# Kernel tuning notes

Measured on AMD Instinct MI355X. Metric: run time of the kernel, lower is better.

## Reference

```python
import jax, jax.numpy as jnp
import numpy as np

B, T, DE, DD, A, FN, FS = 32, 2000, 512, 1024, 128, 32, 16
TEMPERATURE = 1.0


def setup_inputs() -> dict:
    key = jax.random.key(0)
    ks = jax.random.split(key, 10)
    input_enc = jax.random.normal(ks[0], (B, T, DE), dtype=jnp.float32)
    # lengths in [T//2, T] so no zero-length utterances
    enc_lengths = jax.random.randint(ks[1], (B,), T // 2, T + 1, dtype=jnp.int32)
    input_dec = jax.random.normal(ks[2], (B, DD), dtype=jnp.float32)
    # prev_att: previous-step attention weights (masked, normalized)
    prev_att = jax.random.uniform(ks[3], (B, T), dtype=jnp.float32)
    pad = jnp.arange(T)[None, :] >= enc_lengths[:, None]
    prev_att = jnp.where(pad, 0.0, prev_att)
    prev_att = prev_att / jnp.sum(prev_att, axis=1, keepdims=True)
    # parameters
    conv_w = jax.random.normal(ks[4], (FN, 1, 2 * FS + 1), dtype=jnp.float32) * 0.1  # [out,in,k]
    enc_w = jax.random.normal(ks[5], (A, DE), dtype=jnp.float32) * 0.04
    dec_w = jax.random.normal(ks[6], (A, DD), dtype=jnp.float32) * 0.03
    att_w = jax.random.normal(ks[7], (A, FN), dtype=jnp.float32) * 0.17
    att_b = jnp.zeros((A,), dtype=jnp.float32)
    out_w = jax.random.normal(ks[8], (1, A), dtype=jnp.float32) * 0.09
    return dict(input_enc=input_enc, enc_lengths=enc_lengths, input_dec=input_dec,
                prev_att=prev_att, conv_w=conv_w, enc_w=enc_w, dec_w=dec_w,
                att_w=att_w, att_b=att_b, out_w=out_w)


def reference(input_enc, enc_lengths, input_dec, prev_att,
              conv_w, enc_w, dec_w, att_w, att_b, out_w):
    b, t, _ = input_enc.shape
    fs = (conv_w.shape[-1] - 1) // 2  # 'same' padding
    # padding mask: True at padded positions t >= length
    mask = jnp.arange(t)[None, :] >= enc_lengths[:, None]  # [B,T]
    # location features: Conv1d over prev attention, 1 -> FN channels, same length
    conv = jax.lax.conv_general_dilated(
        prev_att[:, None, :], conv_w, window_strides=(1,),
        padding=[(fs, fs)], dimension_numbers=("NCH", "OIH", "NCH"))  # [B,FN,T]
    loc_feat = conv.transpose(0, 2, 1)  # [B,T,FN]
    projected_att = loc_feat @ att_w.T + att_b        # [B,T,A]
    projected_enc = input_enc @ enc_w.T               # [B,T,A]
    projected_dec = (input_dec @ dec_w.T)[:, None, :]  # [B,1,A]
    score = jnp.squeeze(jnp.tanh(projected_att + projected_enc + projected_dec) @ out_w.T, -1)  # [B,T]
    score = jnp.where(mask, -jnp.inf, score)
    att_weight = jax.nn.softmax(TEMPERATURE * score, axis=1)  # [B,T]
    context = jnp.einsum("btd,bt->bd", input_enc, att_weight)  # [B,DE]
    return context, att_weight
```

## Files before the change

### kernel.cpp

```cpp
#include <hip/hip_runtime.h>
#include <hip/hip_bf16.h>
#include <math.h>

#define B_ 32
#define T_ 2000
#define DE_ 512
#define DD_ 1024
#define A_ 128
#define FN_ 32
#define FS_ 16
#define KW_ (2*FS_+1)

typedef __bf16 bf16x8 __attribute__((ext_vector_type(8)));
typedef __bf16 bf16x4 __attribute__((ext_vector_type(4)));
typedef float f32x4 __attribute__((ext_vector_type(4)));

#define BT 64
#define LSTR 40

__device__ __forceinline__ void load_lds16(const void* g, void* l) {
    __builtin_amdgcn_global_load_lds(
        (const __attribute__((address_space(1))) unsigned int*)g,
        (__attribute__((address_space(3))) unsigned int*)l, 16, 0, 0);
}

__device__ __forceinline__ bf16x8 cvt8v(f32x4 x, f32x4 y) {
    bf16x8 o;
    o[0] = (__bf16)x[0]; o[1] = (__bf16)x[1]; o[2] = (__bf16)x[2]; o[3] = (__bf16)x[3];
    o[4] = (__bf16)y[0]; o[5] = (__bf16)y[1]; o[6] = (__bf16)y[2]; o[7] = (__bf16)y[3];
    return o;
}

__global__ __launch_bounds__(256) void prep_kernel(
    const float* __restrict__ enc_w, const float* __restrict__ att_w,
    const float* __restrict__ input_dec, const float* __restrict__ dec_w,
    const float* __restrict__ att_b,
    __bf16* __restrict__ enc_bf, __bf16* __restrict__ att_bf,
    float* __restrict__ pdec, float* __restrict__ ctx_un )
{
    int bx = blockIdx.x, tid = threadIdx.x;
    if (bx < 64) {
        int i = bx * 256 + tid;
        float4 v = ((const float4*)enc_w)[i];
        bf16x4 o;
        o[0] = (__bf16)v.x; o[1] = (__bf16)v.y; o[2] = (__bf16)v.z; o[3] = (__bf16)v.w;
        *(bf16x4*)(enc_bf + (size_t)i * 4) = o;
        if (i < (A_ * FN_) / 4) {
            float4 w = ((const float4*)att_w)[i];
            bf16x4 p;
            p[0] = (__bf16)w.x; p[1] = (__bf16)w.y; p[2] = (__bf16)w.z; p[3] = (__bf16)w.w;
            *(bf16x4*)(att_bf + (size_t)i * 4) = p;
        }
    } else if (bx < 192) {
        int pb = bx - 64;
        int b  = pb >> 2;
        int a0 = (pb & 3) * 32;
        int al = tid >> 3;
        int kg = tid & 7;
        int a  = a0 + al;
        const float4* w = (const float4*)(dec_w + (size_t)a * DD_);
        const float4* x = (const float4*)(input_dec + (size_t)b * DD_);
        float acc = 0.f;
        #pragma unroll 8
        for (int j = 0; j < 32; j++) {
            int i4 = kg + j * 8;
            float4 wv = w[i4], xv = x[i4];
            acc += wv.x * xv.x + wv.y * xv.y + wv.z * xv.z + wv.w * xv.w;
        }
        acc += __shfl_xor(acc, 1, 64);
        acc += __shfl_xor(acc, 2, 64);
        acc += __shfl_xor(acc, 4, 64);
        if (kg == 0) pdec[b * A_ + a] = acc + att_b[a];
    } else {
        int idx = (bx - 192) * 256 + tid;
        if (idx < (B_ * DE_ + B_) / 4 + 1)
            ((float4*)ctx_un)[idx] = make_float4(0.f, 0.f, 0.f, 0.f);
    }
}

__global__ __launch_bounds__(256, 2) void score_kernel(
    const float* __restrict__ input_enc, const __bf16* __restrict__ enc_bf,
    const float* __restrict__ prev_att,  const float* __restrict__ conv_w,
    const __bf16* __restrict__ att_bf,   const float* __restrict__ pdec,
    const float* __restrict__ out_w,     const int* __restrict__ lengths,
    float* __restrict__ wbuf, float* __restrict__ ctx_un,
    float* __restrict__ denom)
{
    __shared__ __align__(16) char At[2][16384];
    __shared__ __align__(16) char Bt[2][16384];
    __shared__ __align__(16) float pa_s[BT + 2 * FS_];
    __shared__ __align__(16) __bf16 loc_s[BT * LSTR];
    __shared__ float w_s[BT];

    const int tid  = threadIdx.x;
    const int lane = tid & 63;
    const int wv   = tid >> 6;
    const int b  = blockIdx.y;
    const int t0 = blockIdx.x * BT;
    const int len = lengths[b];

    auto issueA = [&](int kc, int bufi) {
        #pragma unroll
        for (int j = 0; j < 4; j++) {
            int s  = j * 256 + tid;
            int r  = s >> 4;
            int q  = s & 15;
            int cl = q ^ (r & 15);
            int t  = t0 + r; if (t > T_ - 1) t = T_ - 1;
            load_lds16(input_enc + ((size_t)(b * T_ + t)) * DE_ + kc + cl * 4,
                       At[bufi] + j * 4096 + wv * 1024);
        }
    };
    auto issueB = [&](int kc, int bufi) {
        #pragma unroll
        for (int j = 0; j < 4; j++) {
            int s  = j * 256 + tid;
            int r  = s >> 3;
            int cp = s & 7;
            int c  = cp ^ (r & 7);
            load_lds16(enc_bf + (size_t)r * DE_ + kc + c * 8,
                       Bt[bufi] + j * 4096 + wv * 1024);
        }
    };

    issueA(0, 0);  issueB(0, 0);
    issueA(64, 1); issueB(64, 1);

    const int f    = tid & 31;
    const int rblk = tid >> 5;
    float cwr[KW_];
    #pragma unroll
    for (int k = 0; k < KW_; k++) cwr[k] = conv_w[f * KW_ + k];

    if (tid < BT + 2 * FS_) {
        int t = t0 - FS_ + tid;
        pa_s[tid] = (t >= 0 && t < T_) ? prev_att[b * T_ + t] : 0.f;
    }
    __syncthreads();

    {
        float par[40];
        #pragma unroll
        for (int j = 0; j < 10; j++)
            *(float4*)&par[j * 4] = *(const float4*)&pa_s[rblk * 8 + j * 4];
        float accv[8] = {0.f, 0.f, 0.f, 0.f, 0.f, 0.f, 0.f, 0.f};
        #pragma unroll
        for (int k = 0; k < KW_; k++) {
            float c = cwr[k];
            #pragma unroll
            for (int j = 0; j < 8; j++) accv[j] += par[j + k] * c;
        }
        #pragma unroll
        for (int j = 0; j < 8; j++)
            loc_s[(rblk * 8 + j) * LSTR + f] = (__bf16)accv[j];
    }
    __syncthreads();

    const int col  = lane & 15;
    const int grp  = lane >> 4;
    const int rowb = wv * 16 + col;
    const int sw   = (col & 7);
    const int key  = rowb & 15;

    f32x4 acc[8];
    const f32x4 zero = (f32x4){0.f, 0.f, 0.f, 0.f};

    {
        bf16x8 afrag = *(const bf16x8*)(loc_s + rowb * LSTR + grp * 8);
        #pragma unroll
        for (int i = 0; i < 8; i++) {
            bf16x8 bfrag = *(const bf16x8*)(att_bf + (size_t)(i * 16 + col) * FN_ + grp * 8);
            acc[i] = __builtin_amdgcn_mfma_f32_16x16x32_bf16(afrag, bfrag, zero, 0, 0, 0);
        }
    }

    auto compute = [&](const char* Ab, const char* Bb) {
        f32x4 v0 = *(const f32x4*)(Ab + rowb * 256 + ((grp * 2)     ^ key) * 16);
        f32x4 v1 = *(const f32x4*)(Ab + rowb * 256 + ((grp * 2 + 1) ^ key) * 16);
        f32x4 v2 = *(const f32x4*)(Ab + rowb * 256 + ((8 + grp * 2)     ^ key) * 16);
        f32x4 v3 = *(const f32x4*)(Ab + rowb * 256 + ((8 + grp * 2 + 1) ^ key) * 16);
        bf16x8 af0 = cvt8v(v0, v1);
        bf16x8 af1 = cvt8v(v2, v3);
        #pragma unroll
        for (int i = 0; i < 8; i++) {
            bf16x8 bfrag = *(const bf16x8*)(Bb + (i * 16 + col) * 128 + ((grp ^ sw) * 16));
            acc[i] = __builtin_amdgcn_mfma_f32_16x16x32_bf16(af0, bfrag, acc[i], 0, 0, 0);
        }
        #pragma unroll
        for (int i = 0; i < 8; i++) {
            bf16x8 bfrag = *(const bf16x8*)(Bb + (i * 16 + col) * 128 + (((4 + grp) ^ sw) * 16));
            acc[i] = __builtin_amdgcn_mfma_f32_16x16x32_bf16(af1, bfrag, acc[i], 0, 0, 0);
        }
    };

    #pragma unroll
    for (int it = 0; it < 8; ++it) {
        compute(At[it & 1], Bt[it & 1]);
        if (it == 7) break;
        __builtin_amdgcn_s_barrier();
        if (it + 2 < 8) {
            issueA((it + 2) * 64, it & 1);
            issueB((it + 2) * 64, it & 1);
            asm volatile("s_waitcnt vmcnt(8)" ::: "memory");
        } else {
            asm volatile("s_waitcnt vmcnt(0)" ::: "memory");
        }
        __builtin_amdgcn_s_barrier();
        __builtin_amdgcn_sched_barrier(0);
    }

    float s[4] = {0.f, 0.f, 0.f, 0.f};
    float Mabs = 0.f;
    #pragma unroll
    for (int i = 0; i < 8; i++) {
        int a = i * 16 + col;
        float ow = out_w[a];
        Mabs += fabsf(ow);
        float bias = pdec[b * A_ + a];
        #pragma unroll
        for (int r = 0; r < 4; r++) {
            float v = acc[i][r] + bias;
            v = fminf(fmaxf(v, -15.f), 15.f);
            float e = __expf(2.f * v);
            s[r] += ow * ((e - 1.f) / (e + 1.f));
        }
    }
    #pragma unroll
    for (int r = 0; r < 4; r++) {
        s[r] += __shfl_xor(s[r], 1, 64);
        s[r] += __shfl_xor(s[r], 2, 64);
        s[r] += __shfl_xor(s[r], 4, 64);
        s[r] += __shfl_xor(s[r], 8, 64);
    }
    Mabs += __shfl_xor(Mabs, 1, 64);
    Mabs += __shfl_xor(Mabs, 2, 64);
    Mabs += __shfl_xor(Mabs, 4, 64);
    Mabs += __shfl_xor(Mabs, 8, 64);

    if (col == 0) {
        #pragma unroll
        for (int r = 0; r < 4; r++) {
            int rl = wv * 16 + grp * 4 + r;
            int t = t0 + rl;
            float w = 0.f;
            if (t < len) w = __expf(s[r] - Mabs);
            w_s[rl] = w;
            if (t < T_) wbuf[b * T_ + t] = w;
        }
    }
    __syncthreads();

    if (tid < 64) {
        float w = w_s[tid];
        w += __shfl_xor(w, 1, 64);
        w += __shfl_xor(w, 2, 64);
        w += __shfl_xor(w, 4, 64);
        w += __shfl_xor(w, 8, 64);
        w += __shfl_xor(w, 16, 64);
        w += __shfl_xor(w, 32, 64);
        if (tid == 0) atomicAdd(&denom[b], w);
    }

    int n_eff = len - t0;
    if (n_eff > BT) n_eff = BT;
    if (n_eff > 0) {
        int d0 = tid * 2;
        const float* ebase = input_enc + ((size_t)(b * T_ + t0)) * DE_ + d0;
        float cx = 0.f, cy = 0.f;
        #pragma unroll 8
        for (int t = 0; t < n_eff; t++) {
            float w = w_s[t];
            float2 v = *(const float2*)(ebase + (size_t)t * DE_);
            cx += w * v.x;
            cy += w * v.y;
        }
        atomicAdd(&ctx_un[b * DE_ + d0 + 0], cx);
        atomicAdd(&ctx_un[b * DE_ + d0 + 1], cy);
    }
}

__global__ __launch_bounds__(256) void finalize_kernel(
    const float* __restrict__ wbuf, const float* __restrict__ ctx_un,
    const float* __restrict__ denom, float* __restrict__ out)
{
    int bx = blockIdx.x, tid = threadIdx.x;
    if (bx < 64) {
        int i4 = bx * 256 + tid;
        if (i4 < (B_ * T_) / 4) {
            int b = i4 / (T_ / 4);
            float inv = 1.f / denom[b];
            float4 w = ((const float4*)wbuf)[i4];
            w.x *= inv; w.y *= inv; w.z *= inv; w.w *= inv;
            ((float4*)(out + B_ * DE_))[i4] = w;
        }
    } else {
        int j = (bx - 64) * 256 + tid;
        int b = j / (DE_ / 4);
        float inv = 1.f / denom[b];
        float4 c = ((const float4*)ctx_un)[j];
        c.x *= inv; c.y *= inv; c.z *= inv; c.w *= inv;
        ((float4*)out)[j] = c;
    }
}

extern "C" void kernel_launch(void* const* d_in, const int* in_sizes, int n_in,
                              void* d_out, int out_size, void* d_ws, size_t ws_size,
                              hipStream_t stream)
{
    const float* input_enc   = (const float*)d_in[0];
    const int*   enc_lengths = (const int*)d_in[1];
    const float* input_dec   = (const float*)d_in[2];
    const float* prev_att    = (const float*)d_in[3];
    const float* conv_w      = (const float*)d_in[4];
    const float* enc_w       = (const float*)d_in[5];
    const float* dec_w       = (const float*)d_in[6];
    const float* att_w       = (const float*)d_in[7];
    const float* att_b       = (const float*)d_in[8];
    const float* out_w       = (const float*)d_in[9];

    float* out = (float*)d_out;
    char* ws = (char*)d_ws;
    float*  pdec   = (float*)ws;
    float*  wbuf   = (float*)(ws + 16384);
    __bf16* enc_bf = (__bf16*)(ws + 272384);
    __bf16* att_bf = (__bf16*)(ws + 403456);
    float*  ctx_un = (float*)(ws + 411648);
    float*  denom  = (float*)(ws + 477184);

    prep_kernel<<<209, 256, 0, stream>>>(enc_w, att_w, input_dec, dec_w, att_b,
                                         enc_bf, att_bf, pdec, ctx_un);

    dim3 sgrid((T_ + BT - 1) / BT, B_);
    score_kernel<<<sgrid, 256, 0, stream>>>(input_enc, enc_bf, prev_att, conv_w,
                                            att_bf, pdec, out_w, enc_lengths,
                                            wbuf, ctx_un, denom);

    finalize_kernel<<<80, 256, 0, stream>>>(wbuf, ctx_un, denom, out);
}
```

Measured before the change: 224.9 us.

## Halve K-chunk to 32, raise occupancy to 4 blocks, skip fully padded tiles

The LDS staging chunk for the encoder projection GEMM shrinks from 64 to 32 columns, halving LDS per block, and launch bounds now allow 4 blocks per CU. Swizzle patterns and the pipelined loop are reworked for the smaller tiles, with twice as many iterations and barriers. Blocks whose tile lies entirely beyond the utterance length now write zero weights and exit early, avoiding the GEMM on padded rows. The risks are more synchronization per unit of work, register pressure under the tighter launch bound, and possible mismatch with the unseen epilogue, which may expect every block to contribute to the denominator and context accumulation.

```diff
diff --git a/kernel.cpp b/kernel.cpp
--- a/kernel.cpp
+++ b/kernel.cpp
@@ -16,6 +16,7 @@
 typedef float f32x4 __attribute__((ext_vector_type(4)));
 
 #define BT 64
+#define KC 32
 #define LSTR 40
 
 __device__ __forceinline__ void load_lds16(const void* g, void* l) {
@@ -78,7 +79,7 @@
     }
 }
 
-__global__ __launch_bounds__(256, 2) void score_kernel(
+__global__ __launch_bounds__(256, 4) void score_kernel(
     const float* __restrict__ input_enc, const __bf16* __restrict__ enc_bf,
     const float* __restrict__ prev_att,  const float* __restrict__ conv_w,
     const __bf16* __restrict__ att_bf,   const float* __restrict__ pdec,
@@ -86,8 +87,8 @@
     float* __restrict__ wbuf, float* __restrict__ ctx_un,
     float* __restrict__ denom)
 {
-    __shared__ __align__(16) char At[2][16384];
-    __shared__ __align__(16) char Bt[2][16384];
+    __shared__ __align__(16) char At[2][8192];
+    __shared__ __align__(16) char Bt[2][8192];
     __shared__ __align__(16) float pa_s[BT + 2 * FS_];
     __shared__ __align__(16) __bf16 loc_s[BT * LSTR];
     __shared__ float w_s[BT];
@@ -99,13 +100,21 @@
     const int t0 = blockIdx.x * BT;
     const int len = lengths[b];
 
+    if (t0 >= len) {
+        if (tid < BT) {
+            int t = t0 + tid;
+            if (t < T_) wbuf[b * T_ + t] = 0.f;
+        }
+        return;
+    }
+
     auto issueA = [&](int kc, int bufi) {
         #pragma unroll
-        for (int j = 0; j < 4; j++) {
+        for (int j = 0; j < 2; j++) {
             int s  = j * 256 + tid;
-            int r  = s >> 4;
-            int q  = s & 15;
-            int cl = q ^ (r & 15);
+            int r  = s >> 3;
+            int q  = s & 7;
+            int cl = q ^ (r & 7);
             int t  = t0 + r; if (t > T_ - 1) t = T_ - 1;
             load_lds16(input_enc + ((size_t)(b * T_ + t)) * DE_ + kc + cl * 4,
                        At[bufi] + j * 4096 + wv * 1024);
@@ -113,18 +122,18 @@
     };
     auto issueB = [&](int kc, int bufi) {
         #pragma unroll
-        for (int j = 0; j < 4; j++) {
+        for (int j = 0; j < 2; j++) {
             int s  = j * 256 + tid;
-            int r  = s >> 3;
-            int cp = s & 7;
-            int c  = cp ^ (r & 7);
-            load_lds16(enc_bf + (size_t)r * DE_ + kc + c * 8,
+            int r  = s >> 2;
+            int q  = s & 3;
+            int cl = q ^ ((r >> 1) & 3);
+            load_lds16(enc_bf + (size_t)r * DE_ + kc + cl * 8,
                        Bt[bufi] + j * 4096 + wv * 1024);
         }
     };
 
-    issueA(0, 0);  issueB(0, 0);
-    issueA(64, 1); issueB(64, 1);
+    issueA(0, 0);   issueB(0, 0);
+    issueA(KC, 1);  issueB(KC, 1);
 
     const int f    = tid & 31;
     const int rblk = tid >> 5;
@@ -159,8 +168,7 @@
     const int col  = lane & 15;
     const int grp  = lane >> 4;
     const int rowb = wv * 16 + col;
-    const int sw   = (col & 7);
-    const int key  = rowb & 15;
+    const int keyA = rowb & 7;
 
     f32x4 acc[8];
     const f32x4 zero = (f32x4){0.f, 0.f, 0.f, 0.f};
@@ -175,38 +183,30 @@
     }
 
     auto compute = [&](const char* Ab, const char* Bb) {
-        f32x4 v0 = *(const f32x4*)(Ab + rowb * 256 + ((grp * 2)     ^ key) * 16);
-        f32x4 v1 = *(const f32x4*)(Ab + rowb * 256 + ((grp * 2 + 1) ^ key) * 16);
-        f32x4 v2 = *(const f32x4*)(Ab + rowb * 256 + ((8 + grp * 2)     ^ key) * 16);
-        f32x4 v3 = *(const f32x4*)(Ab + rowb * 256 + ((8 + grp * 2 + 1) ^ key) * 16);
-        bf16x8 af0 = cvt8v(v0, v1);
-        bf16x8 af1 = cvt8v(v2, v3);
+        f32x4 v0 = *(const f32x4*)(Ab + rowb * 128 + ((grp * 2)     ^ keyA) * 16);
+        f32x4 v1 = *(const f32x4*)(Ab + rowb * 128 + ((grp * 2 + 1) ^ keyA) * 16);
+        bf16x8 af = cvt8v(v0, v1);
         #pragma unroll
         for (int i = 0; i < 8; i++) {
-            bf16x8 bfrag = *(const bf16x8*)(Bb + (i * 16 + col) * 128 + ((grp ^ sw) * 16));
-            acc[i] = __builtin_amdgcn_mfma_f32_16x16x32_bf16(af0, bfrag, acc[i], 0, 0, 0);
-        }
-        #pragma unroll
-        for (int i = 0; i < 8; i++) {
-            bf16x8 bfrag = *(const bf16x8*)(Bb + (i * 16 + col) * 128 + (((4 + grp) ^ sw) * 16));
-            acc[i] = __builtin_amdgcn_mfma_f32_16x16x32_bf16(af1, bfrag, acc[i], 0, 0, 0);
+            int row = i * 16 + col;
+            bf16x8 bfrag = *(const bf16x8*)(Bb + row * 64 + ((grp ^ ((row >> 1) & 3)) * 16));
+            acc[i] = __builtin_amdgcn_mfma_f32_16x16x32_bf16(af, bfrag, acc[i], 0, 0, 0);
         }
     };
 
     #pragma unroll
-    for (int it = 0; it < 8; ++it) {
+    for (int it = 0; it < 16; ++it) {
         compute(At[it & 1], Bt[it & 1]);
-        if (it == 7) break;
+        if (it == 15) break;
         __builtin_amdgcn_s_barrier();
-        if (it + 2 < 8) {
-            issueA((it + 2) * 64, it & 1);
-            issueB((it + 2) * 64, it & 1);
-            asm volatile("s_waitcnt vmcnt(8)" ::: "memory");
+        if (it + 2 < 16) {
+            issueA((it + 2) * KC, it & 1);
+            issueB((it + 2) * KC, it & 1);
+            asm volatile("s_waitcnt vmcnt(4)" ::: "memory");
         } else {
             asm volatile("s_waitcnt vmcnt(0)" ::: "memory");
         }
         __builtin_amdgcn_s_barrier();
-        __builtin_amdgcn_sched_barrier(0);
     }
 
     float s[4] = {0.f, 0.f, 0.f, 0.f};
```

Result: no change. 223.8 us (median of 2 runs) (-0.5%).
